# Optimization experiments

Hardware: AMD Instinct MI355X
Metric: run time of the kernel (lower is better)

## Reference

```python
import jax, jax.numpy as jnp
import numpy as np


def setup_inputs() -> dict:
    key = jax.random.key(0)
    k1, k2 = jax.random.split(key)
    # x: (B, C, D, H, W); w: (out_ch, C * 2*2*2)
    x = jax.random.normal(k1, (4, 64, 33, 33, 33), dtype=jnp.float32)
    w = jax.random.normal(k2, (128, 64 * 8), dtype=jnp.float32) * 0.05
    return {"x": x, "w": w}


def reference(x, w):
    # unfoldNd(kernel=2, stride=1, pad=0) + einsum('ij,kjm->kim', w, patches)
    # is exactly a valid 3D cross-correlation with a 2x2x2 kernel.
    B, C, D, H, W = x.shape
    O = w.shape[0]
    kern = w.reshape(O, C, 2, 2, 2)  # unfold flattening order: (C, kd, kh, kw)
    y = jax.lax.conv_general_dilated(
        x, kern,
        window_strides=(1, 1, 1),
        padding='VALID',
        dimension_numbers=('NCDHW', 'OIDHW', 'NCDHW'),
    )  # (B, O, D-1, H-1, W-1)
    return (y + 1.0) ** 2
```

## Files before the change

kernel.cpp:

```cpp
#include <hip/hip_runtime.h>

typedef __bf16 bf16x8 __attribute__((ext_vector_type(8)));
typedef float f32x4 __attribute__((ext_vector_type(4)));
typedef unsigned short u16;
typedef unsigned int u32;
typedef u32 u32x4 __attribute__((ext_vector_type(4)));
typedef u16 u16x8 __attribute__((ext_vector_type(8)));

#define AS1 __attribute__((address_space(1)))
#define AS3 __attribute__((address_space(3)))
#define GLL16(gp, lp) __builtin_amdgcn_global_load_lds((const AS1 void*)(gp), (AS3 void*)(lp), 16, 0, 0)

__device__ __forceinline__ u16 f32_to_bf16_rne(float f) {
    union { float f; unsigned u; } cv; cv.f = f;
    unsigned u = cv.u;
    return (u16)((u + 0x7FFFu + ((u >> 16) & 1u)) >> 16);
}

__device__ __forceinline__ u32 cvt_pk_bf16(float lo, float hi) {
    u32 r;
    asm("v_cvt_pk_bf16_f32 %0, %1, %2" : "=v"(r) : "v"(lo), "v"(hi));
    return r;
}

__global__ void repack_w_kernel(const float* __restrict__ w, u16* __restrict__ w3) {
    int e = blockIdx.x * 256 + threadIdx.x;
    int j    = e & 7;
    int g    = (e >> 3) & 3;
    int o    = (e >> 5) & 127;
    int cb   = (e >> 12) & 1;
    int koff = (e >> 13) & 7;
    int c = (cb << 5) + (g << 3) + j;
    w3[e] = f32_to_bf16_rne(w[(o << 9) + (c << 3) + koff]);
}

__global__ __launch_bounds__(256) void transpose_x_kernel(
    const float* __restrict__ x, u16* __restrict__ xT, u16* __restrict__ x32) {

    const int bid = blockIdx.x;
    const int h = bid % 33;
    const int dq = bid / 33;
    const int d = dq % 33;
    const int b = dq / 33;
    const float* xp = x + (size_t)b * 2299968 + d * 1089 + h * 33;

    const int tid = threadIdx.x;
    const int wv  = tid & 31;
    const int cc  = tid >> 5;
    const float* p = xp + (size_t)cc * 8 * 35937 + wv;
    float f0 = p[0],              f1 = p[35937],          f2 = p[2 * 35937], f3 = p[3 * 35937];
    float f4 = p[(size_t)4*35937],f5 = p[(size_t)5*35937],f6 = p[(size_t)6*35937],f7 = p[(size_t)7*35937];
    u32x4 v;
    v[0] = cvt_pk_bf16(f0, f1);
    v[1] = cvt_pk_bf16(f2, f3);
    v[2] = cvt_pk_bf16(f4, f5);
    v[3] = cvt_pk_bf16(f6, f7);
    *reinterpret_cast<u32x4*>(&xT[(size_t)bid * 2048 + cc * 256 + wv * 8]) = v;

    if (tid < 8) {
        const float* q = xp + (size_t)tid * 8 * 35937 + 32;
        u32x4 m;
        m[0] = cvt_pk_bf16(q[0],              q[35937]);
        m[1] = cvt_pk_bf16(q[2 * 35937],      q[3 * 35937]);
        m[2] = cvt_pk_bf16(q[(size_t)4*35937],q[(size_t)5*35937]);
        m[3] = cvt_pk_bf16(q[(size_t)6*35937],q[(size_t)7*35937]);
        *reinterpret_cast<u32x4*>(&x32[(size_t)bid * 64 + tid * 8]) = m;
    }
}

__global__ __launch_bounds__(512, 4) void conv_mfma_kernel(
    const u16* __restrict__ xT, const u16* __restrict__ x32,
    const u16* __restrict__ w3, float* __restrict__ out) {

    __shared__ __align__(16) u16 xs[19008];

    const int tid = threadIdx.x;
    const int bid = blockIdx.x;
    const int hy0 = (bid & 15) << 1;
    const int dz0 = ((bid >> 4) & 15) << 1;
    const int b   = bid >> 8;

    char* ldsb = (char*)xs;
    const int slab0 = b * 1089 + dz0 * 33 + hy0;
#pragma unroll
    for (int r = 0; r < 5; ++r) {
        if (r == 4 && tid >= 256) continue;
        const int u   = tid + (r << 9);
        const int sid = u >> 8;
        const int s   = (sid * 171) >> 9;
        const int hh  = sid - s * 3;
        const char* src = (const char*)xT + ((size_t)(slab0 + s * 33 + hh) << 12)
                          + ((u & 255) << 4);
        GLL16(src, ldsb + (u << 4));
    }
    if (tid < 72) {
        const int s  = (tid * 171) >> 12;
        const int rr = tid - s * 24;
        const char* src = (const char*)x32
            + ((size_t)(b * 1089 + (dz0 + s) * 33 + hy0) << 7) + (rr << 4);
        GLL16(src, ldsb + 36864 + (tid << 4));
    }
    asm volatile("s_waitcnt vmcnt(0)" ::: "memory");
    __syncthreads();

    const int lane = tid & 63;
    const int ln   = lane & 15;
    const int g    = lane >> 4;
    const int o0   = (tid >> 6) << 4;

    f32x4 acc0[4], acc1[4];
#pragma unroll
    for (int mf = 0; mf < 4; ++mf) {
        acc0[mf] = (f32x4){0.f, 0.f, 0.f, 0.f};
        acc1[mf] = (f32x4){0.f, 0.f, 0.f, 0.f};
    }

#pragma unroll
    for (int cb = 0; cb < 2; ++cb) {
        const int cc = (cb << 2) + g;
        bf16x8 wfA[4], wfB[4];
#pragma unroll
        for (int kk = 0; kk < 4; ++kk) {
            const u16* p = w3 + ((size_t)(((kk << 1) + cb) * 128 + o0 + ln) << 5) + (g << 3);
            wfA[kk] = __builtin_bit_cast(bf16x8, *reinterpret_cast<const u16x8*>(p));
        }
#pragma unroll
        for (int s = 0; s < 3; ++s) {
            if (s == 1) {
#pragma unroll
                for (int kk = 0; kk < 4; ++kk) {
                    const u16* p = w3 + ((size_t)((((4 + kk) << 1) + cb) * 128 + o0 + ln) << 5) + (g << 3);
                    wfB[kk] = __builtin_bit_cast(bf16x8, *reinterpret_cast<const u16x8*>(p));
                }
            }
#pragma unroll
            for (int kw = 0; kw < 2; ++kw) {
                bf16x8 xf[3][2];
#pragma unroll
                for (int hh = 0; hh < 3; ++hh)
#pragma unroll
                    for (int wh = 0; wh < 2; ++wh) {
                        const int row = (wh << 4) + ln + kw;
                        const u16* p = (row < 32)
                            ? &xs[((s * 3 + hh) << 11) + (cc << 8) + (row << 3)]
                            : &xs[18432 + s * 192 + hh * 64 + (cc << 3)];
                        xf[hh][wh] = __builtin_bit_cast(bf16x8,
                            *reinterpret_cast<const u16x8*>(p));
                    }
#pragma unroll
                for (int kh = 0; kh < 2; ++kh) {
                    const int kk = (kh << 1) + kw;
#pragma unroll
                    for (int mf = 0; mf < 4; ++mf) {
                        const bf16x8 xv = xf[(mf >> 1) + kh][mf & 1];
                        if (s < 2)
                            acc0[mf] = __builtin_amdgcn_mfma_f32_16x16x32_bf16(
                                (s == 0 ? wfA : wfB)[kk], xv, acc0[mf], 0, 0, 0);
                        if (s >= 1)
                            acc1[mf] = __builtin_amdgcn_mfma_f32_16x16x32_bf16(
                                (s == 1 ? wfA : wfB)[kk], xv, acc1[mf], 0, 0, 0);
                    }
                }
            }
        }
    }

    float* ob = out + (size_t)b * 128 * 32768 + ((size_t)dz0 << 10) + (hy0 << 5);
#pragma unroll
    for (int mf = 0; mf < 4; ++mf) {
        const int wx   = ((mf & 1) << 4) + ln;
        const int hrow = mf >> 1;
#pragma unroll
        for (int r = 0; r < 4; ++r) {
            const int n = o0 + (g << 2) + r;
            float* o2 = ob + ((size_t)n << 15) + (hrow << 5) + wx;
            float v0 = acc0[mf][r] + 1.0f;
            o2[0] = v0 * v0;
            float v1 = acc1[mf][r] + 1.0f;
            o2[1024] = v1 * v1;
        }
    }
}

#define XS_ROW 72
__global__ __launch_bounds__(256, 4) void conv_mfma_fallback(
    const float* __restrict__ x, const u16* __restrict__ w3, float* __restrict__ out) {

    __shared__ __align__(16) u16 xs[6 * 33 * XS_ROW];

    const int tid = threadIdx.x;
    const int bid = blockIdx.x;
    const int hy0 = (bid & 15) << 1;
    const int dz  = (bid >> 4) & 31;
    const int b   = bid >> 9;

    const float* xb = x + (size_t)b * 64 * 35937;
    for (int i = tid; i < 1584; i += 256) {
        int w   = i % 33;
        int t   = i / 33;
        int q   = t & 7;
        int kh3 = t >> 3;
        int kd  = kh3 >= 3 ? 1 : 0;
        int kh  = kh3 - kd * 3;
        const float* p = xb + (size_t)(q << 3) * 35937 + (dz + kd) * 1089 + (hy0 + kh) * 33 + w;
        u32x4 v;
        v[0] = cvt_pk_bf16(p[0], p[35937]);
        v[1] = cvt_pk_bf16(p[2 * 35937], p[3 * 35937]);
        v[2] = cvt_pk_bf16(p[4 * 35937], p[5 * 35937]);
        v[3] = cvt_pk_bf16(p[6 * 35937], p[7 * 35937]);
        *reinterpret_cast<u32x4*>(&xs[(kh3 * 33 + w) * XS_ROW + (q << 3)]) = v;
    }
    __syncthreads();

    const int lane = tid & 63;
    const int ln   = lane & 15;
    const int g    = lane >> 4;
    const int n0w  = (tid >> 6) << 5;

    f32x4 acc[2][4];
#pragma unroll
    for (int nf = 0; nf < 2; ++nf)
#pragma unroll
        for (int mf = 0; mf < 4; ++mf)
            acc[nf][mf] = (f32x4){0.f, 0.f, 0.f, 0.f};

#pragma unroll
    for (int cb = 0; cb < 2; ++cb) {
        const int cbase = (cb << 5) + (g << 3);
#pragma unroll
        for (int kd = 0; kd < 2; ++kd) {
            bf16x8 wf[2][4];
#pragma unroll
            for (int nf = 0; nf < 2; ++nf)
#pragma unroll
                for (int kk = 0; kk < 4; ++kk) {
                    const int koff = (kd << 2) + kk;
                    const u16* p = w3 + (size_t)((((koff << 1) + cb) << 7)
                                   + n0w + (nf << 4) + ln) * 32 + (g << 3);
                    wf[nf][kk] = __builtin_bit_cast(bf16x8, *reinterpret_cast<const u16x8*>(p));
                }
#pragma unroll
            for (int kw = 0; kw < 2; ++kw) {
                bf16x8 xf[3][2];
#pragma unroll
                for (int hh = 0; hh < 3; ++hh)
#pragma unroll
                    for (int wh = 0; wh < 2; ++wh) {
                        const int row = (kd * 3 + hh) * 33 + (wh << 4) + ln + kw;
                        xf[hh][wh] = __builtin_bit_cast(bf16x8,
                            *reinterpret_cast<const u16x8*>(&xs[row * XS_ROW + cbase]));
                    }
#pragma unroll
                for (int kh = 0; kh < 2; ++kh)
#pragma unroll
                    for (int nf = 0; nf < 2; ++nf)
#pragma unroll
                        for (int mf = 0; mf < 4; ++mf)
                            acc[nf][mf] = __builtin_amdgcn_mfma_f32_16x16x32_bf16(
                                wf[nf][(kh << 1) + kw], xf[(mf >> 1) + kh][mf & 1],
                                acc[nf][mf], 0, 0, 0);
            }
        }
    }

    float* ob = out + ((size_t)b * 128) * 32768 + (dz << 10) + (hy0 << 5);
#pragma unroll
    for (int nf = 0; nf < 2; ++nf)
#pragma unroll
        for (int mf = 0; mf < 4; ++mf) {
            const int wx   = ((mf & 1) << 4) + ln;
            const int hrow = mf >> 1;
            float* o2 = ob + (hrow << 5) + wx;
#pragma unroll
            for (int r = 0; r < 4; ++r) {
                const int n = n0w + (nf << 4) + (g << 2) + r;
                float v = acc[nf][mf][r] + 1.0f;
                o2[(size_t)n << 15] = v * v;
            }
        }
}

extern "C" void kernel_launch(void* const* d_in, const int* in_sizes, int n_in,
                              void* d_out, int out_size, void* d_ws, size_t ws_size,
                              hipStream_t stream) {
    const float* x = (const float*)d_in[0];
    const float* w = (const float*)d_in[1];
    float* out = (float*)d_out;

    const size_t W3_BYTES  = 131072;
    const size_t XT_BYTES  = (size_t)4356 * 4096;
    const size_t X32_BYTES = (size_t)4356 * 128;
    const size_t NEED = W3_BYTES + XT_BYTES + X32_BYTES;

    u16* w3 = (u16*)d_ws;
    repack_w_kernel<<<256, 256, 0, stream>>>(w, w3);

    if (ws_size >= NEED) {
        u16* xT  = (u16*)((char*)d_ws + W3_BYTES);
        u16* x32 = (u16*)((char*)d_ws + W3_BYTES + XT_BYTES);
        transpose_x_kernel<<<4356, 256, 0, stream>>>(x, xT, x32);
        conv_mfma_kernel<<<1024, 512, 0, stream>>>(xT, x32, w3, out);
    } else {
        conv_mfma_fallback<<<2048, 256, 0, stream>>>(x, w3, out);
    }
}
```

Measured before the change: 47.31 us.

## Compute four output depth slices per block to reuse staged input slabs

Each block now computes four output depth planes instead of two. It stages five input depth slabs in LDS (up from three) and keeps 16 accumulator tiles. The grid halves to 512 blocks. This cuts redundant halo loads of input slabs across blocks and amortises the weight fragment loads, at the cost of more LDS and registers per block, which may lower occupancy. With only 512 blocks the GPU may also be less well filled.

```diff
diff --git a/kernel.cpp b/kernel.cpp
--- a/kernel.cpp
+++ b/kernel.cpp
@@ -72,19 +72,19 @@
     const u16* __restrict__ xT, const u16* __restrict__ x32,
     const u16* __restrict__ w3, float* __restrict__ out) {
 
-    __shared__ __align__(16) u16 xs[19008];
+    __shared__ __align__(16) u16 xs[31680];
 
     const int tid = threadIdx.x;
     const int bid = blockIdx.x;
     const int hy0 = (bid & 15) << 1;
-    const int dz0 = ((bid >> 4) & 15) << 1;
-    const int b   = bid >> 8;
+    const int dz0 = ((bid >> 4) & 7) << 2;
+    const int b   = bid >> 7;
 
     char* ldsb = (char*)xs;
     const int slab0 = b * 1089 + dz0 * 33 + hy0;
 #pragma unroll
-    for (int r = 0; r < 5; ++r) {
-        if (r == 4 && tid >= 256) continue;
+    for (int r = 0; r < 8; ++r) {
+        if (r == 7 && tid >= 256) continue;
         const int u   = tid + (r << 9);
         const int sid = u >> 8;
         const int s   = (sid * 171) >> 9;
@@ -93,12 +93,12 @@
                           + ((u & 255) << 4);
         GLL16(src, ldsb + (u << 4));
     }
-    if (tid < 72) {
+    if (tid < 120) {
         const int s  = (tid * 171) >> 12;
         const int rr = tid - s * 24;
         const char* src = (const char*)x32
             + ((size_t)(b * 1089 + (dz0 + s) * 33 + hy0) << 7) + (rr << 4);
-        GLL16(src, ldsb + 36864 + (tid << 4));
+        GLL16(src, ldsb + 61440 + (tid << 4));
     }
     asm volatile("s_waitcnt vmcnt(0)" ::: "memory");
     __syncthreads();
@@ -108,12 +108,12 @@
     const int g    = lane >> 4;
     const int o0   = (tid >> 6) << 4;
 
-    f32x4 acc0[4], acc1[4];
-#pragma unroll
-    for (int mf = 0; mf < 4; ++mf) {
-        acc0[mf] = (f32x4){0.f, 0.f, 0.f, 0.f};
-        acc1[mf] = (f32x4){0.f, 0.f, 0.f, 0.f};
-    }
+    f32x4 acc[4][4];
+#pragma unroll
+    for (int od = 0; od < 4; ++od)
+#pragma unroll
+        for (int mf = 0; mf < 4; ++mf)
+            acc[od][mf] = (f32x4){0.f, 0.f, 0.f, 0.f};
 
 #pragma unroll
     for (int cb = 0; cb < 2; ++cb) {
@@ -125,7 +125,7 @@
             wfA[kk] = __builtin_bit_cast(bf16x8, *reinterpret_cast<const u16x8*>(p));
         }
 #pragma unroll
-        for (int s = 0; s < 3; ++s) {
+        for (int s = 0; s < 5; ++s) {
             if (s == 1) {
 #pragma unroll
                 for (int kk = 0; kk < 4; ++kk) {
@@ -135,30 +135,33 @@
             }
 #pragma unroll
             for (int kw = 0; kw < 2; ++kw) {
-                bf16x8 xf[3][2];
-#pragma unroll
-                for (int hh = 0; hh < 3; ++hh)
+#pragma unroll
+                for (int hh = 0; hh < 3; ++hh) {
+                    bf16x8 xf[2];
 #pragma unroll
                     for (int wh = 0; wh < 2; ++wh) {
                         const int row = (wh << 4) + ln + kw;
                         const u16* p = (row < 32)
                             ? &xs[((s * 3 + hh) << 11) + (cc << 8) + (row << 3)]
-                            : &xs[18432 + s * 192 + hh * 64 + (cc << 3)];
-                        xf[hh][wh] = __builtin_bit_cast(bf16x8,
+                            : &xs[30720 + s * 192 + hh * 64 + (cc << 3)];
+                        xf[wh] = __builtin_bit_cast(bf16x8,
                             *reinterpret_cast<const u16x8*>(p));
                     }
 #pragma unroll
-                for (int kh = 0; kh < 2; ++kh) {
-                    const int kk = (kh << 1) + kw;
-#pragma unroll
-                    for (int mf = 0; mf < 4; ++mf) {
-                        const bf16x8 xv = xf[(mf >> 1) + kh][mf & 1];
-                        if (s < 2)
-                            acc0[mf] = __builtin_amdgcn_mfma_f32_16x16x32_bf16(
-                                (s == 0 ? wfA : wfB)[kk], xv, acc0[mf], 0, 0, 0);
-                        if (s >= 1)
-                            acc1[mf] = __builtin_amdgcn_mfma_f32_16x16x32_bf16(
-                                (s == 1 ? wfA : wfB)[kk], xv, acc1[mf], 0, 0, 0);
+                    for (int kh = 0; kh < 2; ++kh) {
+                        const int hrow = hh - kh;
+                        if (hrow < 0 || hrow > 1) continue;
+                        const int kk = (kh << 1) + kw;
+#pragma unroll
+                        for (int wh = 0; wh < 2; ++wh) {
+                            const int mf = (hrow << 1) + wh;
+                            if (s < 4)
+                                acc[s][mf] = __builtin_amdgcn_mfma_f32_16x16x32_bf16(
+                                    wfA[kk], xf[wh], acc[s][mf], 0, 0, 0);
+                            if (s >= 1)
+                                acc[s - 1][mf] = __builtin_amdgcn_mfma_f32_16x16x32_bf16(
+                                    wfB[kk], xf[wh], acc[s - 1][mf], 0, 0, 0);
+                        }
                     }
                 }
             }
@@ -174,10 +177,11 @@
         for (int r = 0; r < 4; ++r) {
             const int n = o0 + (g << 2) + r;
             float* o2 = ob + ((size_t)n << 15) + (hrow << 5) + wx;
-            float v0 = acc0[mf][r] + 1.0f;
-            o2[0] = v0 * v0;
-            float v1 = acc1[mf][r] + 1.0f;
-            o2[1024] = v1 * v1;
+#pragma unroll
+            for (int od = 0; od < 4; ++od) {
+                float v = acc[od][mf][r] + 1.0f;
+                o2[od << 10] = v * v;
+            }
         }
     }
 }
@@ -299,7 +303,7 @@
         u16* xT  = (u16*)((char*)d_ws + W3_BYTES);
         u16* x32 = (u16*)((char*)d_ws + W3_BYTES + XT_BYTES);
         transpose_x_kernel<<<4356, 256, 0, stream>>>(x, xT, x32);
-        conv_mfma_kernel<<<1024, 512, 0, stream>>>(xT, x32, w3, out);
+        conv_mfma_kernel<<<512, 512, 0, stream>>>(xT, x32, w3, out);
     } else {
         conv_mfma_fallback<<<2048, 256, 0, stream>>>(x, w3, out);
     }
```

Result: faster. 45.87 us (-3.0%).
